# Performance work log

Hardware: AMD Instinct MI355X
Metric: run time of the kernel (lower is better)

## Reference

```python
import jax, jax.numpy as jnp
import numpy as np


def _gcn_conv(x, src, dst, W, b, n):
    """PyG-style GCNConv: symmetric-normalized aggregation with self-loops.
    out = D^{-1/2} (A + I) D^{-1/2} X W + b, deg computed with self-loops.
    """
    xw = x @ W  # [n, out]
    ones = jnp.ones(src.shape[0], dtype=x.dtype)
    deg = jax.ops.segment_sum(ones, dst, num_segments=n) + 1.0  # +1 self-loop
    dinv = jax.lax.rsqrt(deg)
    coef = dinv[src] * dinv[dst]  # [E]
    msg = xw[src] * coef[:, None]  # [E, out] gather + scale
    agg = jax.ops.segment_sum(msg, dst, num_segments=n)
    agg = agg + xw * (dinv * dinv)[:, None]  # self-loop term, norm = 1/deg
    return agg + b


def setup_inputs() -> dict:
    key = jax.random.key(0)
    ks = jax.random.split(key, 7)
    N, E = 500000, 8000000
    x = jax.random.normal(ks[0], (N, 2), dtype=jnp.float32)
    y1 = jax.random.normal(ks[1], (N,), dtype=jnp.float32)
    edge_index = jax.random.randint(ks[2], (2, E), 0, N, dtype=jnp.int64)
    s = 0.2
    W1 = jax.random.normal(ks[3], (3, 29), dtype=jnp.float32) * s
    b1 = jnp.zeros((29,), dtype=jnp.float32)
    W2 = jax.random.normal(ks[4], (32, 29), dtype=jnp.float32) * s
    b2 = jnp.zeros((29,), dtype=jnp.float32)
    W3 = jax.random.normal(ks[5], (32, 1), dtype=jnp.float32) * s
    b3 = jnp.zeros((1,), dtype=jnp.float32)
    return {"x": x, "y1": y1, "edge_index": edge_index,
            "W1": W1, "b1": b1, "W2": W2, "b2": b2, "W3": W3, "b3": b3}


def reference(x, y1, edge_index, W1, b1, W2, b2, W3, b3):
    n = x.shape[0]
    src, dst = edge_index[0], edge_index[1]
    inp = jnp.concatenate([x, y1[:, None]], axis=1)  # [N, 3]
    h = jax.nn.relu(_gcn_conv(inp, src, dst, W1, b1, n))  # [N, 29]
    h = jnp.concatenate([h, inp], axis=1)  # [N, 32] skip
    h = jax.nn.relu(_gcn_conv(h, src, dst, W2, b2, n))  # [N, 29]
    h = jnp.concatenate([h, inp], axis=1)  # [N, 32] skip
    h = _gcn_conv(h, src, dst, W3, b3, n)  # [N, 1]
    return h.reshape(-1)
```

## Files before the change

### kernel.cpp

```cpp
#include <hip/hip_runtime.h>
#include <hip/hip_fp16.h>


#define CAPB       17920
#define BSH2       10
#define BN2        1024
#define PACK_SHIFT 19
#define PACK_MASK  0x7FFFFu
#define SPLIT_CH   8192
#define CAPQ       9216

typedef int v4i __attribute__((ext_vector_type(4)));

__global__ __launch_bounds__(512) void split_kernel(
    const int* __restrict__ src, const int* __restrict__ dst,
    unsigned int* __restrict__ gcur, unsigned int* __restrict__ ebuf, int E) {
    __shared__ unsigned int hist[512];
    __shared__ unsigned int scn[512];
    __shared__ unsigned int delta[512];
    __shared__ unsigned int tots;
    __shared__ unsigned int staged[SPLIT_CH];
    __shared__ unsigned short bid[SPLIT_CH];
    int tid = threadIdx.x;
    long long base = (long long)blockIdx.x * SPLIT_CH;
    hist[tid] = 0;
    __syncthreads();
    unsigned int s[16], d[16];
    if (base + SPLIT_CH <= E) {
        const v4i* s4 = (const v4i*)(src + base);
        const v4i* d4 = (const v4i*)(dst + base);
#pragma unroll
        for (int i = 0; i < 4; i++) {
            v4i sv = __builtin_nontemporal_load(s4 + tid + 512 * i);
            v4i dv = __builtin_nontemporal_load(d4 + tid + 512 * i);
            s[4 * i + 0] = (unsigned int)sv.x; d[4 * i + 0] = (unsigned int)dv.x;
            s[4 * i + 1] = (unsigned int)sv.y; d[4 * i + 1] = (unsigned int)dv.y;
            s[4 * i + 2] = (unsigned int)sv.z; d[4 * i + 2] = (unsigned int)dv.z;
            s[4 * i + 3] = (unsigned int)sv.w; d[4 * i + 3] = (unsigned int)dv.w;
        }
#pragma unroll
        for (int i = 0; i < 16; i++) atomicAdd(&hist[d[i] >> BSH2], 1u);
    } else {
#pragma unroll
        for (int i = 0; i < 16; i++) {
            long long e = base + tid + 512 * i;
            bool ok = e < E;
            s[i] = ok ? (unsigned int)src[e] : 0u;
            d[i] = ok ? (unsigned int)dst[e] : 0xFFFFFFFFu;
            if (ok) atomicAdd(&hist[d[i] >> BSH2], 1u);
        }
    }
    __syncthreads();
    unsigned int c = hist[tid];
    scn[tid] = c; __syncthreads();
    for (int off = 1; off < 512; off <<= 1) {
        unsigned int t = (tid >= off) ? scn[tid - off] : 0u;
        __syncthreads();
        scn[tid] += t;
        __syncthreads();
    }
    unsigned int excl = scn[tid] - c;
    if (tid == 511) tots = scn[511];
    unsigned int gb = c ? atomicAdd(&gcur[tid], c) : 0u;
    delta[tid] = gb - excl;
    hist[tid] = excl;
    __syncthreads();
#pragma unroll
    for (int i = 0; i < 16; i++) {
        if (d[i] != 0xFFFFFFFFu) {
            unsigned int bb = d[i] >> BSH2;
            unsigned int pos = atomicAdd(&hist[bb], 1u);
            staged[pos] = s[i] | ((d[i] & (BN2 - 1)) << PACK_SHIFT);
            bid[pos] = (unsigned short)bb;
        }
    }
    __syncthreads();
    unsigned int tot = tots;
    for (unsigned int i = tid; i < tot; i += 512) {
        unsigned int bb = bid[i];
        unsigned int rel = delta[bb] + i;
        if (rel < CAPB) ebuf[(size_t)bb * CAPB + rel] = staged[i];
    }
}

__global__ __launch_bounds__(1024) void build1_kernel(
    const unsigned int* __restrict__ gcur, const unsigned int* __restrict__ ebuf,
    const float* __restrict__ x, const float* __restrict__ y1,
    unsigned int* __restrict__ rowdeg, float4* __restrict__ u0,
    uint2* __restrict__ u0h, int N) {
    __shared__ unsigned int hist[BN2];
    __shared__ unsigned int aux[1024];
    int b = blockIdx.x, tid = threadIdx.x;
    hist[tid] = 0;
    unsigned int T = gcur[b]; if (T > CAPB) T = CAPB;
    const unsigned int* seg = ebuf + (size_t)b * CAPB;
    __syncthreads();
    for (unsigned int f = tid; f < T; f += 1024)
        atomicAdd(&hist[__builtin_nontemporal_load(seg + f) >> PACK_SHIFT], 1u);
    __syncthreads();
    unsigned int cnt = hist[tid];
    aux[tid] = cnt; __syncthreads();
    for (int off = 1; off < 1024; off <<= 1) {
        unsigned int t = (tid >= off) ? aux[tid - off] : 0u;
        __syncthreads();
        aux[tid] += t;
        __syncthreads();
    }
    unsigned int base = aux[tid] - cnt;
    int n = (b << BSH2) + tid;
    if (n < N) {
        rowdeg[n] = base | (cnt << 16);
        float di = rsqrtf((float)cnt + 1.0f);
        float v0 = x[2 * n] * di, v1 = x[2 * n + 1] * di, v2 = y1[n] * di;
        u0[n] = make_float4(v0, v1, v2, di);
        union { __half2 h2[2]; uint2 u; } pk;
        pk.h2[0] = __floats2half2_rn(v0, v1);
        pk.h2[1] = __floats2half2_rn(v2, 0.f);
        u0h[n] = pk.u;
    }
}

__device__ __forceinline__ unsigned int sfetch(const unsigned int* dest,
                                               const unsigned int* seg2,
                                               unsigned int j, unsigned int dbase) {
    unsigned int loc = j - dbase;
    return (loc < CAPQ) ? dest[loc] : seg2[j];
}

__global__ __launch_bounds__(1024) void build2_kernel(
    const unsigned int* __restrict__ gcur, const unsigned int* __restrict__ ebuf,
    const unsigned int* __restrict__ rowdeg, const float4* __restrict__ u0,
    const uint2* __restrict__ u0h,
    const float* __restrict__ W1, const float* __restrict__ b1,
    unsigned int* __restrict__ ebuf2, uint4* __restrict__ h1s, int N) {
    __shared__ unsigned int cur[BN2];
    __shared__ unsigned int base2[BN2 + 1];
    __shared__ unsigned int dest[CAPQ];
    int b = blockIdx.x, tid = threadIdx.x;
    int gn0 = (b << BSH2);
    int n = gn0 + tid;
    unsigned int T = gcur[b]; if (T > CAPB) T = CAPB;
    unsigned int off = (n < N) ? (rowdeg[n] & 0xFFFFu) : T;
    cur[tid] = off; base2[tid] = off;
    if (tid == 0) base2[BN2] = T;
    const unsigned int* seg = ebuf + (size_t)b * CAPB;
    unsigned int* seg2 = ebuf2 + (size_t)b * CAPB;
    __syncthreads();
    unsigned int qs1 = base2[512];
#pragma unroll 1
    for (int h = 0; h < 2; h++) {
        unsigned int dbase = h ? qs1 : 0;
        for (unsigned int f = tid; f < T; f += 1024) {
            unsigned int p = seg[f];
            unsigned int dloc = p >> PACK_SHIFT;
            if ((int)(dloc >> 9) == h) {
                unsigned int pos = atomicAdd(&cur[dloc], 1u);
                unsigned int s = p & PACK_MASK;
                unsigned int loc = pos - dbase;
                if (loc < CAPQ) dest[loc] = s;
                else            seg2[pos] = s;
            }
        }
        __syncthreads();
        unsigned int hend = h ? T : qs1;
        unsigned int m = hend - dbase; if (m > CAPQ) m = CAPQ;
        for (unsigned int i = tid; i < m; i += 1024) seg2[dbase + i] = dest[i];
        int l = (h << 9) + (tid >> 1);
        int q = tid & 1;
        int gn = gn0 + l;
        if (gn < N) {
            unsigned int o = base2[l], e = base2[l + 1];
            unsigned int cnt = e - o;
            unsigned int hcnt = cnt >> 1;
            unsigned int j0 = o + (q ? hcnt : 0), j1 = q ? e : o + hcnt;
            float4 u = u0[gn];
            float sx = q ? 0.f : u.x, sy = q ? 0.f : u.y, sz = q ? 0.f : u.z;
            unsigned int j = j0;
            for (; j + 4 <= j1; j += 4) {
                unsigned int i0 = sfetch(dest, seg2, j,     dbase);
                unsigned int i1 = sfetch(dest, seg2, j + 1, dbase);
                unsigned int i2 = sfetch(dest, seg2, j + 2, dbase);
                unsigned int i3 = sfetch(dest, seg2, j + 3, dbase);
                union { uint2 u; __half2 h[2]; } g0, g1, g2, g3;
                g0.u = u0h[i0]; g1.u = u0h[i1]; g2.u = u0h[i2]; g3.u = u0h[i3];
                float2 a0 = __half22float2(g0.h[0]), c0 = __half22float2(g0.h[1]);
                float2 a1 = __half22float2(g1.h[0]), c1 = __half22float2(g1.h[1]);
                float2 a2 = __half22float2(g2.h[0]), c2 = __half22float2(g2.h[1]);
                float2 a3 = __half22float2(g3.h[0]), c3 = __half22float2(g3.h[1]);
                sx += (a0.x + a1.x) + (a2.x + a3.x);
                sy += (a0.y + a1.y) + (a2.y + a3.y);
                sz += (c0.x + c1.x) + (c2.x + c3.x);
            }
            for (; j < j1; j++) {
                union { uint2 u; __half2 h[2]; } g;
                g.u = u0h[sfetch(dest, seg2, j, dbase)];
                float2 a = __half22float2(g.h[0]);
                sx += a.x; sy += a.y; sz += __half2float(g.h[1].x);
            }
            sx += __shfl_xor(sx, 1, 64);
            sy += __shfl_xor(sy, 1, 64);
            sz += __shfl_xor(sz, 1, 64);
            float di = u.w;
            float a0 = sx * di, a1 = sy * di, a2 = sz * di;
            float hv[16];
#pragma unroll
            for (int i = 0; i < 16; i++) {
                int k = 16 * q + i;
                if (k < 29) {
                    float v = fmaf(a0, W1[k], fmaf(a1, W1[29 + k], fmaf(a2, W1[58 + k], b1[k])));
                    hv[i] = fmaxf(v, 0.0f) * di;
                } else {
                    hv[i] = (k == 29) ? a0 : (k == 30) ? a1 : a2;
                }
            }
            union { __half2 h2[8]; uint4 u4[2]; } pk;
#pragma unroll
            for (int i = 0; i < 8; i++) pk.h2[i] = __floats2half2_rn(hv[2 * i], hv[2 * i + 1]);
            uint4* row = h1s + (size_t)gn * 4 + 2 * q;
            row[0] = pk.u4[0];
            row[1] = pk.u4[1];
        }
        __syncthreads();
    }
}

__device__ __forceinline__ void unpack8(float4 r, float* o) {
    union { float4 f; __half2 h[4]; } u; u.f = r;
    float2 a = __half22float2(u.h[0]); o[0] = a.x; o[1] = a.y;
    float2 b = __half22float2(u.h[1]); o[2] = b.x; o[3] = b.y;
    float2 c = __half22float2(u.h[2]); o[4] = c.x; o[5] = c.y;
    float2 d = __half22float2(u.h[3]); o[6] = d.x; o[7] = d.y;
}

__global__ __launch_bounds__(256) void pull2_kernel(
    const float4* __restrict__ h1f4, const unsigned int* __restrict__ rowdeg,
    const unsigned int* __restrict__ ebuf2, const float4* __restrict__ u0,
    const float* __restrict__ x, const float* __restrict__ y1,
    const float* __restrict__ W2, const float* __restrict__ b2,
    const float* __restrict__ W3, const float* __restrict__ b3,
    __half* __restrict__ zs, float* __restrict__ out, int N) {
    __shared__ float W2l[32 * 29];
    for (int i = threadIdx.x; i < 32 * 29; i += 256) W2l[i] = W2[i];
    int t = blockIdx.x * 256 + threadIdx.x;
    int n = t >> 2, q = t & 3;
    __syncthreads();
    if (n >= N) return;
    unsigned int rd = rowdeg[n];
    const unsigned int* lst = ebuf2 + (size_t)(n >> BSH2) * CAPB + (rd & 0xFFFFu);
    unsigned int cnt = rd >> 16;
    float acc[8] = {0.f, 0.f, 0.f, 0.f, 0.f, 0.f, 0.f, 0.f};
    unsigned int j = 0;
    for (; j + 4 <= cnt; j += 4) {
        unsigned int s0 = lst[j], s1 = lst[j + 1], s2 = lst[j + 2], s3 = lst[j + 3];
        float4 r0 = h1f4[(size_t)s0 * 4 + q];
        float4 r1 = h1f4[(size_t)s1 * 4 + q];
        float4 r2 = h1f4[(size_t)s2 * 4 + q];
        float4 r3 = h1f4[(size_t)s3 * 4 + q];
        float f0[8], f1[8], f2[8], f3[8];
        unpack8(r0, f0); unpack8(r1, f1); unpack8(r2, f2); unpack8(r3, f3);
#pragma unroll
        for (int i = 0; i < 8; i++) acc[i] += (f0[i] + f1[i]) + (f2[i] + f3[i]);
    }
    for (; j < cnt; j++) {
        float4 r0 = h1f4[(size_t)lst[j] * 4 + q];
        float f0[8]; unpack8(r0, f0);
#pragma unroll
        for (int i = 0; i < 8; i++) acc[i] += f0[i];
    }
    float hs[8];
    { float4 rs = h1f4[(size_t)n * 4 + q]; unpack8(rs, hs); }
    float di = u0[n].w;
    float g[8];
#pragma unroll
    for (int i = 0; i < 8; i++) {
        int jj = 8 * q + i;
        g[i] = (jj < 29) ? (acc[i] + hs[i]) * di
                         : hs[i];
    }
    float p29[29];
#pragma unroll
    for (int kk = 0; kk < 29; kk++) p29[kk] = 0.f;
#pragma unroll
    for (int i = 0; i < 8; i++) {
        float gi = g[i];
        const float* wr = &W2l[(8 * q + i) * 29];
#pragma unroll
        for (int kk = 0; kk < 29; kk++) p29[kk] = fmaf(gi, wr[kk], p29[kk]);
    }
#pragma unroll
    for (int kk = 0; kk < 29; kk++) {
        p29[kk] += __shfl_xor(p29[kk], 1, 64);
        p29[kk] += __shfl_xor(p29[kk], 2, 64);
    }
    if (q == 0) {
        float z = 0.0f;
#pragma unroll
        for (int kk = 0; kk < 29; kk++)
            z = fmaf(fmaxf(p29[kk] + b2[kk], 0.0f), W3[kk], z);
        z = fmaf(x[2 * n], W3[29], z);
        z = fmaf(x[2 * n + 1], W3[30], z);
        z = fmaf(y1[n], W3[31], z);
        zs[n]  = __float2half_rn(z * di);
        out[n] = fmaf(z * di, di, b3[0]);
    }
}

__global__ void pull3_kernel(const __half* __restrict__ zs, const float4* __restrict__ u0,
                             const unsigned int* __restrict__ rowdeg,
                             const unsigned int* __restrict__ ebuf2,
                             float* __restrict__ out, int N) {
    int n = blockIdx.x * blockDim.x + threadIdx.x;
    if (n >= N) return;
    unsigned int rd = rowdeg[n];
    const unsigned int* lst = ebuf2 + (size_t)(n >> BSH2) * CAPB + (rd & 0xFFFFu);
    unsigned int cnt = rd >> 16;
    float s = 0.f;
    unsigned int j = 0;
    for (; j + 4 <= cnt; j += 4) {
        unsigned int i0 = __builtin_nontemporal_load(lst + j);
        unsigned int i1 = __builtin_nontemporal_load(lst + j + 1);
        unsigned int i2 = __builtin_nontemporal_load(lst + j + 2);
        unsigned int i3 = __builtin_nontemporal_load(lst + j + 3);
        s += (__half2float(zs[i0]) + __half2float(zs[i1]))
           + (__half2float(zs[i2]) + __half2float(zs[i3]));
    }
    for (; j < cnt; j++) s += __half2float(zs[lst[j]]);
    out[n] += s * u0[n].w;
}

extern "C" void kernel_launch(void* const* d_in, const int* in_sizes, int n_in,
                              void* d_out, int out_size, void* d_ws, size_t ws_size,
                              hipStream_t stream) {
    const float* x  = (const float*)d_in[0];
    const float* y1 = (const float*)d_in[1];
    const int*   ei = (const int*)d_in[2];
    const float* W1 = (const float*)d_in[3];
    const float* b1 = (const float*)d_in[4];
    const float* W2 = (const float*)d_in[5];
    const float* b2 = (const float*)d_in[6];
    const float* W3 = (const float*)d_in[7];
    const float* b3 = (const float*)d_in[8];
    float* out = (float*)d_out;

    int N = in_sizes[1];
    int E = in_sizes[2] / 2;
    const int* src = ei;
    const int* dst = ei + E;

    size_t Ns = (size_t)N;
    int nb = (N + BN2 - 1) >> BSH2;
    size_t segtot = (size_t)512 * CAPB;

    float* ws = (float*)d_ws;
    float4*       u0     = (float4*)ws;
    __half*       zs     = (__half*)(ws + 4 * Ns);
    unsigned int* rowdeg = (unsigned int*)(ws + 5 * Ns);
    uint2*        u0h    = (uint2*)(ws + 6 * Ns);
    unsigned int* gcur   = (unsigned int*)(ws + 8 * Ns);
    unsigned int* ebuf   = gcur + 512;
    unsigned int* ebuf2  = ebuf + segtot;
    uint4*        h1s    = (uint4*)(ebuf2 + segtot);

    hipMemsetAsync(gcur, 0, 512 * sizeof(unsigned int), stream);

    const int gS = (E + SPLIT_CH - 1) / SPLIT_CH;
    const int gN = (N + 255) / 256;
    const int g4 = (4 * N + 255) / 256;
    split_kernel <<<gS, 512, 0, stream>>>(src, dst, gcur, ebuf, E);
    build1_kernel<<<nb, 1024, 0, stream>>>(gcur, ebuf, x, y1, rowdeg, u0, u0h, N);
    build2_kernel<<<nb, 1024, 0, stream>>>(gcur, ebuf, rowdeg, u0, u0h, W1, b1,
                                           ebuf2, h1s, N);
    pull2_kernel <<<g4, 256, 0, stream>>>((const float4*)h1s, rowdeg, ebuf2, u0,
                                          x, y1, W2, b2, W3, b3, zs, out, N);
    pull3_kernel <<<gN, 256, 0, stream>>>(zs, u0, rowdeg, ebuf2, out, N);
}
```

Measured before the change: 458.9 us.

## Sort per-destination neighbor lists by source chunk and grid-stride pull2

build1 now builds an 8-way histogram per destination keyed by the source-index high bits and stores packed per-chunk counts. build2 uses these counts to scatter each destination's neighbors grouped by source range, so later gathers touch memory in a more local order. pull2 becomes a capped grid-stride loop and reads edge indices with nontemporal loads. The cost is an 8x larger shared histogram, which lowers occupancy, plus an extra chunkcnt buffer, and the per-node 8-bit chunk counts could overflow on very high-degree nodes.

```diff
diff --git a/kernel.cpp b/kernel.cpp
--- a/kernel.cpp
+++ b/kernel.cpp
@@ -9,6 +9,7 @@
 #define PACK_MASK  0x7FFFFu
 #define SPLIT_CH   8192
 #define CAPQ       9216
+#define NCH        8
 
 typedef int v4i __attribute__((ext_vector_type(4)));
 
@@ -87,18 +88,22 @@
     const unsigned int* __restrict__ gcur, const unsigned int* __restrict__ ebuf,
     const float* __restrict__ x, const float* __restrict__ y1,
     unsigned int* __restrict__ rowdeg, float4* __restrict__ u0,
-    uint2* __restrict__ u0h, int N) {
-    __shared__ unsigned int hist[BN2];
+    uint2* __restrict__ u0h, uint2* __restrict__ chunkcnt, int N) {
+    __shared__ unsigned int hist[BN2 * NCH];
     __shared__ unsigned int aux[1024];
     int b = blockIdx.x, tid = threadIdx.x;
-    hist[tid] = 0;
+    for (int i = tid; i < BN2 * NCH; i += 1024) hist[i] = 0;
     unsigned int T = gcur[b]; if (T > CAPB) T = CAPB;
     const unsigned int* seg = ebuf + (size_t)b * CAPB;
     __syncthreads();
-    for (unsigned int f = tid; f < T; f += 1024)
-        atomicAdd(&hist[__builtin_nontemporal_load(seg + f) >> PACK_SHIFT], 1u);
-    __syncthreads();
-    unsigned int cnt = hist[tid];
+    for (unsigned int f = tid; f < T; f += 1024) {
+        unsigned int p = __builtin_nontemporal_load(seg + f);
+        atomicAdd(&hist[((p >> PACK_SHIFT) << 3) | ((p & PACK_MASK) >> 16)], 1u);
+    }
+    __syncthreads();
+    unsigned int c8[NCH], cnt = 0;
+#pragma unroll
+    for (int cc = 0; cc < NCH; cc++) { c8[cc] = hist[(tid << 3) | cc]; cnt += c8[cc]; }
     aux[tid] = cnt; __syncthreads();
     for (int off = 1; off < 1024; off <<= 1) {
         unsigned int t = (tid >= off) ? aux[tid - off] : 0u;
@@ -107,6 +112,10 @@
         __syncthreads();
     }
     unsigned int base = aux[tid] - cnt;
+    union { unsigned char c[8]; uint2 u; } pk2;
+#pragma unroll
+    for (int cc = 0; cc < NCH; cc++) pk2.c[cc] = (unsigned char)c8[cc];
+    chunkcnt[(size_t)(b << BSH2) + tid] = pk2.u;
     int n = (b << BSH2) + tid;
     if (n < N) {
         rowdeg[n] = base | (cnt << 16);
@@ -130,10 +139,10 @@
 __global__ __launch_bounds__(1024) void build2_kernel(
     const unsigned int* __restrict__ gcur, const unsigned int* __restrict__ ebuf,
     const unsigned int* __restrict__ rowdeg, const float4* __restrict__ u0,
-    const uint2* __restrict__ u0h,
+    const uint2* __restrict__ u0h, const uint2* __restrict__ chunkcnt,
     const float* __restrict__ W1, const float* __restrict__ b1,
     unsigned int* __restrict__ ebuf2, uint4* __restrict__ h1s, int N) {
-    __shared__ unsigned int cur[BN2];
+    __shared__ unsigned int cur[BN2 * NCH];
     __shared__ unsigned int base2[BN2 + 1];
     __shared__ unsigned int dest[CAPQ];
     int b = blockIdx.x, tid = threadIdx.x;
@@ -141,7 +150,14 @@
     int n = gn0 + tid;
     unsigned int T = gcur[b]; if (T > CAPB) T = CAPB;
     unsigned int off = (n < N) ? (rowdeg[n] & 0xFFFFu) : T;
-    cur[tid] = off; base2[tid] = off;
+    {
+        union { uint2 u; unsigned char c[8]; } ld;
+        ld.u = chunkcnt[(size_t)gn0 + tid];
+        unsigned int r = off;
+#pragma unroll
+        for (int cc = 0; cc < NCH; cc++) { cur[(tid << 3) | cc] = r; r += ld.c[cc]; }
+    }
+    base2[tid] = off;
     if (tid == 0) base2[BN2] = T;
     const unsigned int* seg = ebuf + (size_t)b * CAPB;
     unsigned int* seg2 = ebuf2 + (size_t)b * CAPB;
@@ -154,8 +170,8 @@
             unsigned int p = seg[f];
             unsigned int dloc = p >> PACK_SHIFT;
             if ((int)(dloc >> 9) == h) {
-                unsigned int pos = atomicAdd(&cur[dloc], 1u);
                 unsigned int s = p & PACK_MASK;
+                unsigned int pos = atomicAdd(&cur[(dloc << 3) | (s >> 16)], 1u);
                 unsigned int loc = pos - dbase;
                 if (loc < CAPQ) dest[loc] = s;
                 else            seg2[pos] = s;
@@ -241,67 +257,72 @@
     __half* __restrict__ zs, float* __restrict__ out, int N) {
     __shared__ float W2l[32 * 29];
     for (int i = threadIdx.x; i < 32 * 29; i += 256) W2l[i] = W2[i];
-    int t = blockIdx.x * 256 + threadIdx.x;
-    int n = t >> 2, q = t & 3;
-    __syncthreads();
-    if (n >= N) return;
-    unsigned int rd = rowdeg[n];
-    const unsigned int* lst = ebuf2 + (size_t)(n >> BSH2) * CAPB + (rd & 0xFFFFu);
-    unsigned int cnt = rd >> 16;
-    float acc[8] = {0.f, 0.f, 0.f, 0.f, 0.f, 0.f, 0.f, 0.f};
-    unsigned int j = 0;
-    for (; j + 4 <= cnt; j += 4) {
-        unsigned int s0 = lst[j], s1 = lst[j + 1], s2 = lst[j + 2], s3 = lst[j + 3];
-        float4 r0 = h1f4[(size_t)s0 * 4 + q];
-        float4 r1 = h1f4[(size_t)s1 * 4 + q];
-        float4 r2 = h1f4[(size_t)s2 * 4 + q];
-        float4 r3 = h1f4[(size_t)s3 * 4 + q];
-        float f0[8], f1[8], f2[8], f3[8];
-        unpack8(r0, f0); unpack8(r1, f1); unpack8(r2, f2); unpack8(r3, f3);
-#pragma unroll
-        for (int i = 0; i < 8; i++) acc[i] += (f0[i] + f1[i]) + (f2[i] + f3[i]);
-    }
-    for (; j < cnt; j++) {
-        float4 r0 = h1f4[(size_t)lst[j] * 4 + q];
-        float f0[8]; unpack8(r0, f0);
-#pragma unroll
-        for (int i = 0; i < 8; i++) acc[i] += f0[i];
-    }
-    float hs[8];
-    { float4 rs = h1f4[(size_t)n * 4 + q]; unpack8(rs, hs); }
-    float di = u0[n].w;
-    float g[8];
-#pragma unroll
-    for (int i = 0; i < 8; i++) {
-        int jj = 8 * q + i;
-        g[i] = (jj < 29) ? (acc[i] + hs[i]) * di
-                         : hs[i];
-    }
-    float p29[29];
-#pragma unroll
-    for (int kk = 0; kk < 29; kk++) p29[kk] = 0.f;
-#pragma unroll
-    for (int i = 0; i < 8; i++) {
-        float gi = g[i];
-        const float* wr = &W2l[(8 * q + i) * 29];
-#pragma unroll
-        for (int kk = 0; kk < 29; kk++) p29[kk] = fmaf(gi, wr[kk], p29[kk]);
-    }
-#pragma unroll
-    for (int kk = 0; kk < 29; kk++) {
-        p29[kk] += __shfl_xor(p29[kk], 1, 64);
-        p29[kk] += __shfl_xor(p29[kk], 2, 64);
-    }
-    if (q == 0) {
-        float z = 0.0f;
-#pragma unroll
-        for (int kk = 0; kk < 29; kk++)
-            z = fmaf(fmaxf(p29[kk] + b2[kk], 0.0f), W3[kk], z);
-        z = fmaf(x[2 * n], W3[29], z);
-        z = fmaf(x[2 * n + 1], W3[30], z);
-        z = fmaf(y1[n], W3[31], z);
-        zs[n]  = __float2half_rn(z * di);
-        out[n] = fmaf(z * di, di, b3[0]);
+    __syncthreads();
+    int q = threadIdx.x & 3;
+    int step = gridDim.x * 64;
+    for (int n = blockIdx.x * 64 + (threadIdx.x >> 2); n < N; n += step) {
+        unsigned int rd = rowdeg[n];
+        const unsigned int* lst = ebuf2 + (size_t)(n >> BSH2) * CAPB + (rd & 0xFFFFu);
+        unsigned int cnt = rd >> 16;
+        float acc[8] = {0.f, 0.f, 0.f, 0.f, 0.f, 0.f, 0.f, 0.f};
+        unsigned int j = 0;
+        for (; j + 4 <= cnt; j += 4) {
+            unsigned int s0 = __builtin_nontemporal_load(lst + j);
+            unsigned int s1 = __builtin_nontemporal_load(lst + j + 1);
+            unsigned int s2 = __builtin_nontemporal_load(lst + j + 2);
+            unsigned int s3 = __builtin_nontemporal_load(lst + j + 3);
+            float4 r0 = h1f4[(size_t)s0 * 4 + q];
+            float4 r1 = h1f4[(size_t)s1 * 4 + q];
+            float4 r2 = h1f4[(size_t)s2 * 4 + q];
+            float4 r3 = h1f4[(size_t)s3 * 4 + q];
+            float f0[8], f1[8], f2[8], f3[8];
+            unpack8(r0, f0); unpack8(r1, f1); unpack8(r2, f2); unpack8(r3, f3);
+#pragma unroll
+            for (int i = 0; i < 8; i++) acc[i] += (f0[i] + f1[i]) + (f2[i] + f3[i]);
+        }
+        for (; j < cnt; j++) {
+            unsigned int s0 = __builtin_nontemporal_load(lst + j);
+            float4 r0 = h1f4[(size_t)s0 * 4 + q];
+            float f0[8]; unpack8(r0, f0);
+#pragma unroll
+            for (int i = 0; i < 8; i++) acc[i] += f0[i];
+        }
+        float hs[8];
+        { float4 rs = h1f4[(size_t)n * 4 + q]; unpack8(rs, hs); }
+        float di = u0[n].w;
+        float g[8];
+#pragma unroll
+        for (int i = 0; i < 8; i++) {
+            int jj = 8 * q + i;
+            g[i] = (jj < 29) ? (acc[i] + hs[i]) * di
+                             : hs[i];
+        }
+        float p29[29];
+#pragma unroll
+        for (int kk = 0; kk < 29; kk++) p29[kk] = 0.f;
+#pragma unroll
+        for (int i = 0; i < 8; i++) {
+            float gi = g[i];
+            const float* wr = &W2l[(8 * q + i) * 29];
+#pragma unroll
+            for (int kk = 0; kk < 29; kk++) p29[kk] = fmaf(gi, wr[kk], p29[kk]);
+        }
+#pragma unroll
+        for (int kk = 0; kk < 29; kk++) {
+            p29[kk] += __shfl_xor(p29[kk], 1, 64);
+            p29[kk] += __shfl_xor(p29[kk], 2, 64);
+        }
+        if (q == 0) {
+            float z = 0.0f;
+#pragma unroll
+            for (int kk = 0; kk < 29; kk++)
+                z = fmaf(fmaxf(p29[kk] + b2[kk], 0.0f), W3[kk], z);
+            z = fmaf(x[2 * n], W3[29], z);
+            z = fmaf(x[2 * n + 1], W3[30], z);
+            z = fmaf(y1[n], W3[31], z);
+            zs[n]  = __float2half_rn(z * di);
+            out[n] = fmaf(z * di, di, b3[0]);
+        }
     }
 }
 
@@ -360,17 +381,20 @@
     unsigned int* ebuf   = gcur + 512;
     unsigned int* ebuf2  = ebuf + segtot;
     uint4*        h1s    = (uint4*)(ebuf2 + segtot);
+    uint2*        chunkcnt = (uint2*)(h1s + 4 * Ns);
 
     hipMemsetAsync(gcur, 0, 512 * sizeof(unsigned int), stream);
 
     const int gS = (E + SPLIT_CH - 1) / SPLIT_CH;
     const int gN = (N + 255) / 256;
-    const int g4 = (4 * N + 255) / 256;
+    int gp2 = (N + 63) / 64;
+    if (gp2 > 2048) gp2 = 2048;
     split_kernel <<<gS, 512, 0, stream>>>(src, dst, gcur, ebuf, E);
-    build1_kernel<<<nb, 1024, 0, stream>>>(gcur, ebuf, x, y1, rowdeg, u0, u0h, N);
-    build2_kernel<<<nb, 1024, 0, stream>>>(gcur, ebuf, rowdeg, u0, u0h, W1, b1,
-                                           ebuf2, h1s, N);
-    pull2_kernel <<<g4, 256, 0, stream>>>((const float4*)h1s, rowdeg, ebuf2, u0,
-                                          x, y1, W2, b2, W3, b3, zs, out, N);
+    build1_kernel<<<nb, 1024, 0, stream>>>(gcur, ebuf, x, y1, rowdeg, u0, u0h,
+                                           chunkcnt, N);
+    build2_kernel<<<nb, 1024, 0, stream>>>(gcur, ebuf, rowdeg, u0, u0h, chunkcnt,
+                                           W1, b1, ebuf2, h1s, N);
+    pull2_kernel <<<gp2, 256, 0, stream>>>((const float4*)h1s, rowdeg, ebuf2, u0,
+                                           x, y1, W2, b2, W3, b3, zs, out, N);
     pull3_kernel <<<gN, 256, 0, stream>>>(zs, u0, rowdeg, ebuf2, out, N);
 }
```

Measured after the change: 679.5 us. 48.1% more time.

## Single-pass CSR build in build2 with larger LDS buffer and wave-shuffle scans

Applied to the files above, without the earlier changes.

build2 now sorts all of a bucket's edges into one enlarged LDS destination buffer in a single pass, instead of two half-passes each re-reading the segment. The two node halves are then walked back to back without the barrier between them. The block-wide prefix scans in split and build1 are replaced by wave-level shuffle scans plus a small per-wave fixup, cutting many __syncthreads. The larger LDS allocation (about 68KB plus more) may lower occupancy, and the nontemporal hint on the build1 histogram load is dropped.

```diff
diff --git a/kernel.cpp b/kernel.cpp
--- a/kernel.cpp
+++ b/kernel.cpp
@@ -8,7 +8,7 @@
 #define PACK_SHIFT 19
 #define PACK_MASK  0x7FFFFu
 #define SPLIT_CH   8192
-#define CAPQ       9216
+#define DEST_CAP   17408
 
 typedef int v4i __attribute__((ext_vector_type(4)));
 
@@ -16,8 +16,8 @@
     const int* __restrict__ src, const int* __restrict__ dst,
     unsigned int* __restrict__ gcur, unsigned int* __restrict__ ebuf, int E) {
     __shared__ unsigned int hist[512];
-    __shared__ unsigned int scn[512];
     __shared__ unsigned int delta[512];
+    __shared__ unsigned int wsum[8];
     __shared__ unsigned int tots;
     __shared__ unsigned int staged[SPLIT_CH];
     __shared__ unsigned short bid[SPLIT_CH];
@@ -52,15 +52,23 @@
     }
     __syncthreads();
     unsigned int c = hist[tid];
-    scn[tid] = c; __syncthreads();
-    for (int off = 1; off < 512; off <<= 1) {
-        unsigned int t = (tid >= off) ? scn[tid - off] : 0u;
-        __syncthreads();
-        scn[tid] += t;
-        __syncthreads();
-    }
-    unsigned int excl = scn[tid] - c;
-    if (tid == 511) tots = scn[511];
+    unsigned int v = c;
+#pragma unroll
+    for (int off = 1; off < 64; off <<= 1) {
+        unsigned int t = __shfl_up(v, off, 64);
+        if ((tid & 63) >= off) v += t;
+    }
+    int wv = tid >> 6;
+    if ((tid & 63) == 63) wsum[wv] = v;
+    __syncthreads();
+    if (tid == 0) {
+        unsigned int r = 0;
+#pragma unroll
+        for (int i = 0; i < 8; i++) { unsigned int t = wsum[i]; wsum[i] = r; r += t; }
+        tots = r;
+    }
+    __syncthreads();
+    unsigned int excl = v + wsum[wv] - c;
     unsigned int gb = c ? atomicAdd(&gcur[tid], c) : 0u;
     delta[tid] = gb - excl;
     hist[tid] = excl;
@@ -89,24 +97,32 @@
     unsigned int* __restrict__ rowdeg, float4* __restrict__ u0,
     uint2* __restrict__ u0h, int N) {
     __shared__ unsigned int hist[BN2];
-    __shared__ unsigned int aux[1024];
+    __shared__ unsigned int wsum[16];
     int b = blockIdx.x, tid = threadIdx.x;
     hist[tid] = 0;
     unsigned int T = gcur[b]; if (T > CAPB) T = CAPB;
     const unsigned int* seg = ebuf + (size_t)b * CAPB;
     __syncthreads();
     for (unsigned int f = tid; f < T; f += 1024)
-        atomicAdd(&hist[__builtin_nontemporal_load(seg + f) >> PACK_SHIFT], 1u);
+        atomicAdd(&hist[seg[f] >> PACK_SHIFT], 1u);
     __syncthreads();
     unsigned int cnt = hist[tid];
-    aux[tid] = cnt; __syncthreads();
-    for (int off = 1; off < 1024; off <<= 1) {
-        unsigned int t = (tid >= off) ? aux[tid - off] : 0u;
-        __syncthreads();
-        aux[tid] += t;
-        __syncthreads();
-    }
-    unsigned int base = aux[tid] - cnt;
+    unsigned int v = cnt;
+#pragma unroll
+    for (int off = 1; off < 64; off <<= 1) {
+        unsigned int t = __shfl_up(v, off, 64);
+        if ((tid & 63) >= off) v += t;
+    }
+    int wv = tid >> 6;
+    if ((tid & 63) == 63) wsum[wv] = v;
+    __syncthreads();
+    if (tid == 0) {
+        unsigned int r = 0;
+#pragma unroll
+        for (int i = 0; i < 16; i++) { unsigned int t = wsum[i]; wsum[i] = r; r += t; }
+    }
+    __syncthreads();
+    unsigned int base = v + wsum[wv] - cnt;
     int n = (b << BSH2) + tid;
     if (n < N) {
         rowdeg[n] = base | (cnt << 16);
@@ -120,11 +136,67 @@
     }
 }
 
-__device__ __forceinline__ unsigned int sfetch(const unsigned int* dest,
-                                               const unsigned int* seg2,
-                                               unsigned int j, unsigned int dbase) {
-    unsigned int loc = j - dbase;
-    return (loc < CAPQ) ? dest[loc] : seg2[j];
+__device__ __forceinline__ unsigned int sfetch2(const unsigned int* dest,
+                                                const unsigned int* seg2,
+                                                unsigned int j) {
+    return (j < DEST_CAP) ? dest[j] : seg2[j];
+}
+
+__device__ __forceinline__ void walk_node(
+    int gn, int q, unsigned int o, unsigned int e,
+    const unsigned int* __restrict__ dest, const unsigned int* __restrict__ seg2,
+    const uint2* __restrict__ u0h, const float4* __restrict__ u0,
+    const float* __restrict__ W1, const float* __restrict__ b1,
+    uint4* __restrict__ h1s) {
+    unsigned int cnt = e - o;
+    unsigned int hcnt = cnt >> 1;
+    unsigned int j0 = o + (q ? hcnt : 0), j1 = q ? e : o + hcnt;
+    float4 u = u0[gn];
+    float sx = q ? 0.f : u.x, sy = q ? 0.f : u.y, sz = q ? 0.f : u.z;
+    unsigned int j = j0;
+    for (; j + 4 <= j1; j += 4) {
+        unsigned int i0 = sfetch2(dest, seg2, j);
+        unsigned int i1 = sfetch2(dest, seg2, j + 1);
+        unsigned int i2 = sfetch2(dest, seg2, j + 2);
+        unsigned int i3 = sfetch2(dest, seg2, j + 3);
+        union { uint2 u; __half2 h[2]; } g0, g1, g2, g3;
+        g0.u = u0h[i0]; g1.u = u0h[i1]; g2.u = u0h[i2]; g3.u = u0h[i3];
+        float2 a0 = __half22float2(g0.h[0]), c0 = __half22float2(g0.h[1]);
+        float2 a1 = __half22float2(g1.h[0]), c1 = __half22float2(g1.h[1]);
+        float2 a2 = __half22float2(g2.h[0]), c2 = __half22float2(g2.h[1]);
+        float2 a3 = __half22float2(g3.h[0]), c3 = __half22float2(g3.h[1]);
+        sx += (a0.x + a1.x) + (a2.x + a3.x);
+        sy += (a0.y + a1.y) + (a2.y + a3.y);
+        sz += (c0.x + c1.x) + (c2.x + c3.x);
+    }
+    for (; j < j1; j++) {
+        union { uint2 u; __half2 h[2]; } g;
+        g.u = u0h[sfetch2(dest, seg2, j)];
+        float2 a = __half22float2(g.h[0]);
+        sx += a.x; sy += a.y; sz += __half2float(g.h[1].x);
+    }
+    sx += __shfl_xor(sx, 1, 64);
+    sy += __shfl_xor(sy, 1, 64);
+    sz += __shfl_xor(sz, 1, 64);
+    float di = u.w;
+    float a0 = sx * di, a1 = sy * di, a2 = sz * di;
+    float hv[16];
+#pragma unroll
+    for (int i = 0; i < 16; i++) {
+        int k = 16 * q + i;
+        if (k < 29) {
+            float vv = fmaf(a0, W1[k], fmaf(a1, W1[29 + k], fmaf(a2, W1[58 + k], b1[k])));
+            hv[i] = fmaxf(vv, 0.0f) * di;
+        } else {
+            hv[i] = (k == 29) ? a0 : (k == 30) ? a1 : a2;
+        }
+    }
+    union { __half2 h2[8]; uint4 u4[2]; } pk;
+#pragma unroll
+    for (int i = 0; i < 8; i++) pk.h2[i] = __floats2half2_rn(hv[2 * i], hv[2 * i + 1]);
+    uint4* row = h1s + (size_t)gn * 4 + 2 * q;
+    row[0] = pk.u4[0];
+    row[1] = pk.u4[1];
 }
 
 __global__ __launch_bounds__(1024) void build2_kernel(
@@ -135,7 +207,7 @@
     unsigned int* __restrict__ ebuf2, uint4* __restrict__ h1s, int N) {
     __shared__ unsigned int cur[BN2];
     __shared__ unsigned int base2[BN2 + 1];
-    __shared__ unsigned int dest[CAPQ];
+    __shared__ unsigned int dest[DEST_CAP];
     int b = blockIdx.x, tid = threadIdx.x;
     int gn0 = (b << BSH2);
     int n = gn0 + tid;
@@ -146,82 +218,26 @@
     const unsigned int* seg = ebuf + (size_t)b * CAPB;
     unsigned int* seg2 = ebuf2 + (size_t)b * CAPB;
     __syncthreads();
-    unsigned int qs1 = base2[512];
-#pragma unroll 1
-    for (int h = 0; h < 2; h++) {
-        unsigned int dbase = h ? qs1 : 0;
-        for (unsigned int f = tid; f < T; f += 1024) {
-            unsigned int p = seg[f];
-            unsigned int dloc = p >> PACK_SHIFT;
-            if ((int)(dloc >> 9) == h) {
-                unsigned int pos = atomicAdd(&cur[dloc], 1u);
-                unsigned int s = p & PACK_MASK;
-                unsigned int loc = pos - dbase;
-                if (loc < CAPQ) dest[loc] = s;
-                else            seg2[pos] = s;
-            }
-        }
-        __syncthreads();
-        unsigned int hend = h ? T : qs1;
-        unsigned int m = hend - dbase; if (m > CAPQ) m = CAPQ;
-        for (unsigned int i = tid; i < m; i += 1024) seg2[dbase + i] = dest[i];
-        int l = (h << 9) + (tid >> 1);
-        int q = tid & 1;
-        int gn = gn0 + l;
-        if (gn < N) {
-            unsigned int o = base2[l], e = base2[l + 1];
-            unsigned int cnt = e - o;
-            unsigned int hcnt = cnt >> 1;
-            unsigned int j0 = o + (q ? hcnt : 0), j1 = q ? e : o + hcnt;
-            float4 u = u0[gn];
-            float sx = q ? 0.f : u.x, sy = q ? 0.f : u.y, sz = q ? 0.f : u.z;
-            unsigned int j = j0;
-            for (; j + 4 <= j1; j += 4) {
-                unsigned int i0 = sfetch(dest, seg2, j,     dbase);
-                unsigned int i1 = sfetch(dest, seg2, j + 1, dbase);
-                unsigned int i2 = sfetch(dest, seg2, j + 2, dbase);
-                unsigned int i3 = sfetch(dest, seg2, j + 3, dbase);
-                union { uint2 u; __half2 h[2]; } g0, g1, g2, g3;
-                g0.u = u0h[i0]; g1.u = u0h[i1]; g2.u = u0h[i2]; g3.u = u0h[i3];
-                float2 a0 = __half22float2(g0.h[0]), c0 = __half22float2(g0.h[1]);
-                float2 a1 = __half22float2(g1.h[0]), c1 = __half22float2(g1.h[1]);
-                float2 a2 = __half22float2(g2.h[0]), c2 = __half22float2(g2.h[1]);
-                float2 a3 = __half22float2(g3.h[0]), c3 = __half22float2(g3.h[1]);
-                sx += (a0.x + a1.x) + (a2.x + a3.x);
-                sy += (a0.y + a1.y) + (a2.y + a3.y);
-                sz += (c0.x + c1.x) + (c2.x + c3.x);
-            }
-            for (; j < j1; j++) {
-                union { uint2 u; __half2 h[2]; } g;
-                g.u = u0h[sfetch(dest, seg2, j, dbase)];
-                float2 a = __half22float2(g.h[0]);
-                sx += a.x; sy += a.y; sz += __half2float(g.h[1].x);
-            }
-            sx += __shfl_xor(sx, 1, 64);
-            sy += __shfl_xor(sy, 1, 64);
-            sz += __shfl_xor(sz, 1, 64);
-            float di = u.w;
-            float a0 = sx * di, a1 = sy * di, a2 = sz * di;
-            float hv[16];
-#pragma unroll
-            for (int i = 0; i < 16; i++) {
-                int k = 16 * q + i;
-                if (k < 29) {
-                    float v = fmaf(a0, W1[k], fmaf(a1, W1[29 + k], fmaf(a2, W1[58 + k], b1[k])));
-                    hv[i] = fmaxf(v, 0.0f) * di;
-                } else {
-                    hv[i] = (k == 29) ? a0 : (k == 30) ? a1 : a2;
-                }
-            }
-            union { __half2 h2[8]; uint4 u4[2]; } pk;
-#pragma unroll
-            for (int i = 0; i < 8; i++) pk.h2[i] = __floats2half2_rn(hv[2 * i], hv[2 * i + 1]);
-            uint4* row = h1s + (size_t)gn * 4 + 2 * q;
-            row[0] = pk.u4[0];
-            row[1] = pk.u4[1];
-        }
-        __syncthreads();
-    }
+    for (unsigned int f = tid; f < T; f += 1024) {
+        unsigned int p = seg[f];
+        unsigned int dloc = p >> PACK_SHIFT;
+        unsigned int pos = atomicAdd(&cur[dloc], 1u);
+        unsigned int s = p & PACK_MASK;
+        if (pos < DEST_CAP) dest[pos] = s;
+        else                seg2[pos] = s;
+    }
+    __syncthreads();
+    unsigned int m = T < DEST_CAP ? T : DEST_CAP;
+    for (unsigned int i = tid; i < m; i += 1024) seg2[i] = dest[i];
+    int q = tid & 1;
+    int l0 = tid >> 1;
+    int gnA = gn0 + l0;
+    if (gnA < N)
+        walk_node(gnA, q, base2[l0], base2[l0 + 1], dest, seg2, u0h, u0, W1, b1, h1s);
+    int l1 = l0 + 512;
+    int gnB = gn0 + l1;
+    if (gnB < N)
+        walk_node(gnB, q, base2[l1], base2[l1 + 1], dest, seg2, u0h, u0, W1, b1, h1s);
 }
 
 __device__ __forceinline__ void unpack8(float4 r, float* o) {
```

Result: faster. 431.3 us (-6.0%).
